# Kernel optimization log

Hardware: AMD Instinct MI355X
Metric: run time of the kernel (lower is better)

Reference implementation:

```python
import jax, jax.numpy as jnp
import numpy as np

SF, RES, TS = 8192, 40, 1  # sample freq, resolution (orders), time span (s)


def _eofft(inputs, rpm):
    """Engine-order FFT: per-sample zero-pad to length n_i = L + floor((RES*60/rpm_i - TS)*SF),
    FFT along time, keep first SF bins, take magnitude. Implemented as a fully batched
    Bluestein (chirp-z) transform so every sample uses the SAME fixed FFT size M,
    despite different logical FFT lengths n_i.
    """
    B, L, C = inputs.shape            # L == SF (required by the original .view)
    N = SF * TS                       # nonzero signal length after truncation (8192)
    K = SF                            # number of output bins kept (8192)
    M = int(2 ** np.ceil(np.log2(N + K - 1)))  # 16384, fixed batched FFT size

    x = inputs[:, :N, :]              # truncate, [B, N, C]
    pad = jnp.floor((RES * 60.0 / rpm - TS) * SF).astype(jnp.int32)  # [B]
    n = L + pad                       # per-sample DFT length n_i, [B] int32

    # Phases use exact integer m^2 mod 2n (exp(i*pi*q/n) has period 2n in q),
    # so float32 stays accurate even for large m.
    two_n = (2 * n)[:, None]                              # [B,1]
    nf = n.astype(jnp.float32)[:, None]                   # [B,1]

    # a[t] = x[t] * exp(-i*pi*t^2/n)
    t = jnp.arange(N, dtype=jnp.int32)
    a_phase = jnp.pi * ((t * t) % two_n).astype(jnp.float32) / nf      # [B,N]
    a = x.astype(jnp.complex64) * jnp.exp(-1j * a_phase)[:, :, None]   # [B,N,C]
    a = jnp.pad(a, ((0, 0), (0, M - N), (0, 0)))                       # [B,M,C]

    # b[m] = exp(+i*pi*m^2/n), laid out circularly: index m for m<K, index M-m for m=1..N-1
    m = jnp.arange(M, dtype=jnp.int32)
    mm = jnp.minimum(m, M - m)
    b_phase = jnp.pi * ((mm * mm) % two_n).astype(jnp.float32) / nf    # [B,M]
    b = jnp.exp(1j * b_phase)                                          # [B,M]

    # circular convolution via fixed-size FFTs (batched over B and C)
    conv = jnp.fft.ifft(jnp.fft.fft(a, axis=1) * jnp.fft.fft(b, axis=1)[:, :, None], axis=1)

    # X[k] = exp(-i*pi*k^2/n) * conv[k], k = 0..K-1
    k = jnp.arange(K, dtype=jnp.int32)
    k_phase = jnp.pi * ((k * k) % two_n).astype(jnp.float32) / nf      # [B,K]
    X = jnp.exp(-1j * k_phase)[:, :, None] * conv[:, :K, :]            # [B,K,C]
    return jnp.abs(X)                                                  # [B,SF,C] float32


def setup_inputs() -> dict:
    key = jax.random.key(0)
    k1, k2 = jax.random.split(key)
    B, L, C = 64, 8192, 8
    inputs = jax.random.normal(k1, (B, L, C), dtype=jnp.float32)
    rpm = jax.random.uniform(k2, (B,), dtype=jnp.float32, minval=600.0, maxval=2400.0)
    return {"inputs": inputs, "rpm": rpm}


def reference(inputs, rpm):
    return _eofft(inputs, rpm)
```

## Files before the change

### kernel.cpp

```cpp
#include <hip/hip_runtime.h>
#include <hip/hip_fp16.h>
#include <math.h>


static constexpr int Bn = 64;

#define PI_F 3.14159265358979323846f
#define TWO_PI_F 6.28318530717958647692f
#define R2_F 0.70710678118654752f

__device__ __forceinline__ int compute_n(float rpm) {
    return 8192 + (int)floorf((2400.0f / rpm - 1.0f) * 8192.0f);
}
__device__ __forceinline__ float2 cmul(float2 a, float2 b) {
    return make_float2(a.x*b.x - a.y*b.y, a.x*b.y + a.y*b.x);
}
__device__ __forceinline__ float2 cadd(float2 a, float2 b){ return make_float2(a.x+b.x, a.y+b.y); }
__device__ __forceinline__ float2 csub(float2 a, float2 b){ return make_float2(a.x-b.x, a.y-b.y); }
__device__ __forceinline__ float2 shflx1(float2 v) {
    return make_float2(__shfl_xor(v.x, 1, 64), __shfl_xor(v.y, 1, 64));
}
__device__ __forceinline__ int brev7(int x) { return (int)(__brev((unsigned)x) >> 25); }

#define BF(lo,hi,tw) { float2 _d = csub(lo,hi); lo = cadd(lo,hi); hi = cmul(_d, tw); }
#define BT(lo,hi,tw) { float2 _b = cmul(hi,tw); hi = csub(lo,_b); lo = cadd(lo,_b); }
#define SELC(r,c0,s0,c1,s1) ((r) ? make_float2(c1,s1) : make_float2(c0,s0))
#define IDX(u) ((u) + ((u) >> 4))

__device__ __forceinline__ float2 wtab(const float2* Whi, const float2* Wlo, int m) {
    return cmul(Whi[m >> 7], Wlo[m & 127]);
}

template<bool HZ>
__device__ __forceinline__ void difR(float2 v[8], float2* Lf, int p,
                                     const float2* sWhi) {
    float2 w1 = sWhi[p];
    float2 w2 = cmul(w1, w1);
    float2 w4 = cmul(w2, w2);
    float2 w1b = cmul(w1, make_float2(R2_F,-R2_F));
    float2 w1c = make_float2(w1.y, -w1.x);
    float2 w1d = cmul(w1, make_float2(-R2_F,-R2_F));
    float2 w2i = make_float2(w2.y, -w2.x);
    if (HZ) {
        v[4] = cmul(v[0], w1);
        v[5] = cmul(v[1], w1b);
        v[6] = cmul(v[2], w1c);
        v[7] = cmul(v[3], w1d);
    } else {
        BF(v[0],v[4], w1);
        BF(v[1],v[5], w1b);
        BF(v[2],v[6], w1c);
        BF(v[3],v[7], w1d);
    }
    BF(v[0],v[2], w2);  BF(v[1],v[3], w2i);
    BF(v[4],v[6], w2);  BF(v[5],v[7], w2i);
    BF(v[0],v[1], w4);  BF(v[2],v[3], w4);
    BF(v[4],v[5], w4);  BF(v[6],v[7], w4);
    #pragma unroll
    for (int q = 0; q < 8; ++q) Lf[IDX(p + 16*q)] = v[q];
    int bb = p >> 1, r = p & 1;
    #pragma unroll
    for (int s = 0; s < 8; ++s) v[s] = Lf[IDX(16*bb + r + 2*s)];
    BF(v[0],v[4], SELC(r, 1.f,0.f,                    0.92387953f,-0.38268343f));
    BF(v[1],v[5], SELC(r, 0.70710678f,-0.70710678f,   0.38268343f,-0.92387953f));
    BF(v[2],v[6], SELC(r, 0.f,-1.f,                  -0.38268343f,-0.92387953f));
    BF(v[3],v[7], SELC(r, -0.70710678f,-0.70710678f, -0.92387953f,-0.38268343f));
    BF(v[0],v[2], SELC(r, 1.f,0.f,  0.70710678f,-0.70710678f));
    BF(v[1],v[3], SELC(r, 0.f,-1.f, -0.70710678f,-0.70710678f));
    BF(v[4],v[6], SELC(r, 1.f,0.f,  0.70710678f,-0.70710678f));
    BF(v[5],v[7], SELC(r, 0.f,-1.f, -0.70710678f,-0.70710678f));
    #pragma unroll
    for (int s = 0; s < 8; s += 2) {
        float2 d = csub(v[s], v[s+1]);
        v[s] = cadd(v[s], v[s+1]);
        v[s+1] = r ? make_float2(d.y, -d.x) : d;
    }
    #pragma unroll
    for (int s = 0; s < 8; ++s) {
        float2 o = shflx1(v[s]);
        v[s] = r ? csub(o, v[s]) : cadd(v[s], o);
    }
}

template<bool HOUT>
__device__ __forceinline__ void ditR(float2 v[8], float2* Lf, int p,
                                     const float2* sWhi) {
    int bb = p >> 1, r = p & 1;
    #pragma unroll
    for (int s = 0; s < 8; ++s) {
        float2 o = shflx1(v[s]);
        v[s] = r ? csub(o, v[s]) : cadd(v[s], o);
    }
    #pragma unroll
    for (int s = 0; s < 8; s += 2) {
        float2 bq = v[s+1];
        if (r) bq = make_float2(-bq.y, bq.x);
        v[s+1] = csub(v[s], bq);
        v[s] = cadd(v[s], bq);
    }
    BT(v[0],v[2], SELC(r, 1.f,0.f,  0.70710678f,0.70710678f));
    BT(v[1],v[3], SELC(r, 0.f,1.f, -0.70710678f,0.70710678f));
    BT(v[4],v[6], SELC(r, 1.f,0.f,  0.70710678f,0.70710678f));
    BT(v[5],v[7], SELC(r, 0.f,1.f, -0.70710678f,0.70710678f));
    BT(v[0],v[4], SELC(r, 1.f,0.f,                   0.92387953f,0.38268343f));
    BT(v[1],v[5], SELC(r, 0.70710678f,0.70710678f,   0.38268343f,0.92387953f));
    BT(v[2],v[6], SELC(r, 0.f,1.f,                  -0.38268343f,0.92387953f));
    BT(v[3],v[7], SELC(r, -0.70710678f,0.70710678f, -0.92387953f,0.38268343f));
    #pragma unroll
    for (int s = 0; s < 8; ++s) Lf[IDX(16*bb + r + 2*s)] = v[s];
    #pragma unroll
    for (int q = 0; q < 8; ++q) v[q] = Lf[IDX(p + 16*q)];
    float2 w1 = make_float2(sWhi[p].x, -sWhi[p].y);
    float2 w2 = cmul(w1, w1);
    float2 w4 = cmul(w2, w2);
    float2 w2j = make_float2(-w2.y, w2.x);
    float2 w1b = cmul(w1, make_float2(R2_F, R2_F));
    float2 w1c = make_float2(-w1.y, w1.x);
    float2 w1d = cmul(w1, make_float2(-R2_F, R2_F));
    BT(v[0],v[1], w4); BT(v[2],v[3], w4);
    BT(v[4],v[5], w4); BT(v[6],v[7], w4);
    BT(v[0],v[2], w2);  BT(v[1],v[3], w2j);
    BT(v[4],v[6], w2);  BT(v[5],v[7], w2j);
    if (HOUT) {
        v[0] = cadd(v[0], cmul(v[4], w1));
        v[1] = cadd(v[1], cmul(v[5], w1b));
        v[2] = cadd(v[2], cmul(v[6], w1c));
        v[3] = cadd(v[3], cmul(v[7], w1d));
    } else {
        BT(v[0],v[4], w1);
        BT(v[1],v[5], w1b);
        BT(v[2],v[6], w1c);
        BT(v[3],v[7], w1d);
    }
}

__device__ __forceinline__ void load_tabs(float2* sWhi, float2* sWlo, int tid) {
    if (tid < 128) {
        float sn, cs; __sincosf(PI_F * (float)tid * (1.0f/64.0f), &sn, &cs);
        sWhi[tid] = make_float2(cs, -sn);
    } else if (tid < 256) {
        int m = tid - 128;
        float sn, cs; __sincosf(PI_F * (float)m * (1.0f/8192.0f), &sn, &cs);
        sWlo[m] = make_float2(cs, -sn);
    }
}

__global__ __launch_bounds__(256) void bhat_p1(const float* __restrict__ rpm,
                                               float2* __restrict__ w1c) {
    __shared__ float2 Lw[16 * 137];
    __shared__ float2 sWhi[128];
    __shared__ float2 sWlo[128];
    int tid = threadIdx.x;
    int g = tid >> 4, p = tid & 15;
    int bb = p >> 1, r = p & 1;
    int b = blockIdx.x >> 3;
    int t1_0 = (blockIdx.x & 7) << 4;

    load_tabs(sWhi, sWlo, tid);
    int n = compute_n(rpm[b]);
    int two_n = 2 * n;
    float inv_n = 1.0f / (float)n;
    #pragma unroll
    for (int i = 0; i < 8; ++i) {
        int l = i * 256 + tid;
        int t2 = l >> 4, c = l & 15;
        int t = (t1_0 + c) + (t2 << 7);
        int mm = min(t, 16384 - t);
        int ph = (mm * mm) % two_n;
        float sn, cs; __sincosf(PI_F * (float)ph * inv_n, &sn, &cs);
        Lw[c * 137 + IDX(t2)] = make_float2(cs, sn);
    }
    __syncthreads();
    float2 v[8];
    #pragma unroll
    for (int q = 0; q < 8; ++q) v[q] = Lw[g * 137 + IDX(p + 16*q)];
    difR<false>(v, Lw + g * 137, p, sWhi);
    __syncthreads();
    {
        int t1 = t1_0 + g;
        int k2base = brev7(16*bb + r);
        float2 cur = wtab(sWhi, sWlo, t1 * k2base);
        float2 w8  = wtab(sWhi, sWlo, 8 * t1);
        #pragma unroll
        for (int e = 0; e < 8; ++e) {
            const int s = ((e & 1) << 2) | (e & 2) | ((e & 4) >> 2);
            Lw[(16*bb + r + 2*s) * 17 + g] = cmul(v[s], cur);
            cur = cmul(cur, w8);
        }
    }
    __syncthreads();
    {
        float2* wb = w1c + ((size_t)b << 14) + t1_0;
        #pragma unroll
        for (int i = 0; i < 8; ++i) {
            int l = i * 256 + tid;
            int j = l >> 4, w = l & 15;
            wb[(j << 7) + w] = Lw[j * 17 + w];
        }
    }
}

__global__ __launch_bounds__(256) void k1(const float* __restrict__ x,
                                          const float* __restrict__ rpm,
                                          __half2* __restrict__ w1) {
    __shared__ float2 Lw[16 * 137];
    __shared__ float2 chirpT[128];
    __shared__ float2 sWhi[128];
    __shared__ float2 sWlo[128];
    int tid = threadIdx.x;
    int g = tid >> 4, p = tid & 15;
    int bb = p >> 1, r = p & 1;
    int b = blockIdx.x >> 6;
    int t1_0 = (blockIdx.x & 63) << 1;

    load_tabs(sWhi, sWlo, tid);
    int n = compute_n(rpm[b]);
    int two_n = 2 * n;
    float inv_n = 1.0f / (float)n;
    if (tid < 128) {
        int t2 = tid >> 1, t1l = tid & 1;
        int t = t1_0 + t1l + (t2 << 7);
        int ph = (t * t) % two_n;
        float sn, cs; __sincosf(PI_F * (float)ph * inv_n, &sn, &cs);
        chirpT[tid] = make_float2(cs, -sn);
    }
    __syncthreads();
    {
        const float2* xb2 = (const float2*)(x + ((size_t)b << 16));
        #pragma unroll
        for (int i = 0; i < 2; ++i) {
            int l = i * 256 + tid;
            int t2 = l >> 3, w = l & 7;
            int t1l = w >> 2, cp = w & 3;
            float2 xv = xb2[(size_t)(t1_0 + t1l + (t2 << 7)) * 4 + cp];
            float2 u = chirpT[t2 * 2 + t1l];
            int c = t1l * 8 + cp * 2;
            Lw[c * 137 + IDX(t2)]       = make_float2(xv.x * u.x, xv.x * u.y);
            Lw[(c + 1) * 137 + IDX(t2)] = make_float2(xv.y * u.x, xv.y * u.y);
        }
    }
    __syncthreads();
    float2 v[8];
    #pragma unroll
    for (int q = 0; q < 4; ++q) v[q] = Lw[g * 137 + IDX(p + 16*q)];
    difR<true>(v, Lw + g * 137, p, sWhi);
    __syncthreads();
    {
        int t1 = t1_0 + (g >> 3);
        int k2base = brev7(16*bb + r);
        float2 cur = wtab(sWhi, sWlo, t1 * k2base);
        float2 w8  = wtab(sWhi, sWlo, 8 * t1);
        #pragma unroll
        for (int e = 0; e < 8; ++e) {
            const int s = ((e & 1) << 2) | (e & 2) | ((e & 4) >> 2);
            Lw[(16*bb + r + 2*s) * 17 + g] = cmul(v[s], cur);
            cur = cmul(cur, w8);
        }
    }
    __syncthreads();
    {
        __half2* wb = w1 + ((size_t)b << 17) + (t1_0 << 3);
        #pragma unroll
        for (int i = 0; i < 8; ++i) {
            int l = i * 256 + tid;
            int j = l >> 4, w = l & 15;
            wb[((size_t)j << 10) + w] = __float22half2_rn(Lw[j * 17 + w]);
        }
    }
}

__global__ __launch_bounds__(512) void k2(const __half2* __restrict__ w1,
                                          const float2* __restrict__ w1c,
                                          __half2* __restrict__ s2) {
    __shared__ float2 Lw[32 * 137];
    __shared__ float2 Wsc[4 * 137];
    __shared__ float2 sWhi[128];
    __shared__ float2 sWlo[128];
    int tid = threadIdx.x;
    int g = tid >> 4, p = tid & 15;
    int b = blockIdx.x >> 5;
    int j0 = (blockIdx.x & 31) << 2;

    load_tabs(sWhi, sWlo, tid);
    float2 vb[8];
    if (g < 4) {
        const float2* wc = w1c + ((size_t)b << 14) + ((size_t)(j0 + g) << 7);
        #pragma unroll
        for (int q = 0; q < 8; ++q) vb[q] = wc[p + 16*q];
    }
    {
        const __half2* rb = w1 + ((size_t)b << 17) + ((size_t)j0 << 10);
        #pragma unroll
        for (int i = 0; i < 8; ++i) {
            int l = i * 512 + tid;
            int jl = l >> 10, t1 = (l >> 3) & 127, ch = l & 7;
            Lw[(jl * 8 + ch) * 137 + IDX(t1)] = __half22float2(rb[l]);
        }
    }
    __syncthreads();
    if (g < 4) {
        difR<false>(vb, Wsc + g * 137, p, sWhi);
        #pragma unroll
        for (int s = 0; s < 8; ++s) Wsc[g * 137 + s * 17 + p] = vb[s];
    }
    float2* Lf = Lw + g * 137;
    float2 v[8];
    #pragma unroll
    for (int q = 0; q < 8; ++q) v[q] = Lf[IDX(p + 16*q)];
    difR<false>(v, Lf, p, sWhi);
    __syncthreads();
    {
        int jl = g >> 3;
        #pragma unroll
        for (int s = 0; s < 8; ++s) v[s] = cmul(v[s], Wsc[jl * 137 + s * 17 + p]);
    }
    ditR<false>(v, Lf, p, sWhi);
    int j = j0 + (g >> 3);
    int k2v = brev7(j);
    __syncthreads();
    {
        float2 cur = wtab(sWhi, sWlo, k2v * p);
        float2 w16 = wtab(sWhi, sWlo, 16 * k2v);
        #pragma unroll
        for (int q = 0; q < 8; ++q) {
            float2 tw = make_float2(cur.x * (1.0f/16384.0f), -cur.y * (1.0f/16384.0f));
            Lw[(p + 16*q) * 33 + g] = cmul(v[q], tw);
            cur = cmul(cur, w16);
        }
    }
    __syncthreads();
    {
        __half2* sb = s2 + ((size_t)b << 17) + (j0 << 3);
        #pragma unroll
        for (int i = 0; i < 8; ++i) {
            int l = i * 512 + tid;
            int t1 = l >> 5, w = l & 31;
            sb[((size_t)t1 << 10) + w] = __float22half2_rn(Lw[t1 * 33 + w]);
        }
    }
}

__global__ __launch_bounds__(256) void k3(const __half2* __restrict__ s2,
                                          float* __restrict__ outF) {
    __shared__ float2 Lw[16 * 137];
    __shared__ float2 sWhi[128];
    __shared__ float2 sWlo[128];
    int tid = threadIdx.x;
    int g = tid >> 4, p = tid & 15;
    int bb = p >> 1, r = p & 1;
    int b = blockIdx.x >> 6;
    int t1_0 = (blockIdx.x & 63) << 1;

    load_tabs(sWhi, sWlo, tid);
    {
        const __half2* rb = s2 + ((size_t)b << 17) + ((size_t)t1_0 << 10);
        #pragma unroll
        for (int i = 0; i < 8; ++i) {
            int l = i * 256 + tid;
            int t1l = l >> 10, j = (l >> 3) & 127, ch = l & 7;
            Lw[(t1l * 8 + ch) * 137 + IDX(j)] = __half22float2(rb[l]);
        }
    }
    __syncthreads();
    float2 v[8];
    {
        float2* Lf = Lw + g * 137;
        #pragma unroll
        for (int s = 0; s < 8; ++s) v[s] = Lf[IDX(16*bb + r + 2*s)];
        ditR<true>(v, Lf, p, sWhi);
    }
    __syncthreads();
    float* Lsf = (float*)Lw;
    #pragma unroll
    for (int q = 0; q < 4; ++q) {
        float2 z = v[q];
        Lsf[(p + 16*q) * 20 + g] = sqrtf(z.x*z.x + z.y*z.y);
    }
    __syncthreads();
    {
        float* ob = outF + ((size_t)b << 16) + (t1_0 << 3);
        #pragma unroll
        for (int i = 0; i < 4; ++i) {
            int l = i * 256 + tid;
            int t2 = l >> 4, w = l & 15;
            ob[((size_t)t2 << 10) + w] = Lsf[t2 * 20 + w];
        }
    }
}

extern "C" void kernel_launch(void* const* d_in, const int* in_sizes, int n_in,
                              void* d_out, int out_size, void* d_ws, size_t ws_size,
                              hipStream_t stream) {
    const float* x   = (const float*)d_in[0];
    const float* rpm = (const float*)d_in[1];
    float* outF = (float*)d_out;
    __half2* w1  = (__half2*)d_ws;
    __half2* s2  = w1 + (size_t)Bn * 131072;
    float2* w1c  = (float2*)(s2 + (size_t)Bn * 131072);

    bhat_p1<<<Bn * 8, 256, 0, stream>>>(rpm, w1c);
    k1<<<Bn * 64, 256, 0, stream>>>(x, rpm, w1);
    k2<<<Bn * 32, 512, 0, stream>>>(w1, w1c, s2);
    k3<<<Bn * 64, 256, 0, stream>>>(s2, outF);
}
```

Measured before the change: 76.28 us.

## Merge chirp-FFT kernel into k1 and widen global accesses to float4

New measurement: 70.48 us. 7.6% less time.

```diff
diff --git a/kernel.cpp b/kernel.cpp
--- a/kernel.cpp
+++ b/kernel.cpp
@@ -21,6 +21,17 @@
     return make_float2(__shfl_xor(v.x, 1, 64), __shfl_xor(v.y, 1, 64));
 }
 __device__ __forceinline__ int brev7(int x) { return (int)(__brev((unsigned)x) >> 25); }
+
+__device__ __forceinline__ float f2h_bits(float2 a) {
+    union { __half2 h; float f; } u;
+    u.h = __float22half2_rn(a);
+    return u.f;
+}
+__device__ __forceinline__ float2 h2f_bits(float w) {
+    union { float f; __half2 h; } u;
+    u.f = w;
+    return __half22float2(u.h);
+}
 
 #define BF(lo,hi,tw) { float2 _d = csub(lo,hi); lo = cadd(lo,hi); hi = cmul(_d, tw); }
 #define BT(lo,hi,tw) { float2 _b = cmul(hi,tw); hi = csub(lo,_b); lo = cadd(lo,_b); }
@@ -145,64 +156,10 @@
     }
 }
 
-__global__ __launch_bounds__(256) void bhat_p1(const float* __restrict__ rpm,
-                                               float2* __restrict__ w1c) {
-    __shared__ float2 Lw[16 * 137];
-    __shared__ float2 sWhi[128];
-    __shared__ float2 sWlo[128];
-    int tid = threadIdx.x;
-    int g = tid >> 4, p = tid & 15;
-    int bb = p >> 1, r = p & 1;
-    int b = blockIdx.x >> 3;
-    int t1_0 = (blockIdx.x & 7) << 4;
-
-    load_tabs(sWhi, sWlo, tid);
-    int n = compute_n(rpm[b]);
-    int two_n = 2 * n;
-    float inv_n = 1.0f / (float)n;
-    #pragma unroll
-    for (int i = 0; i < 8; ++i) {
-        int l = i * 256 + tid;
-        int t2 = l >> 4, c = l & 15;
-        int t = (t1_0 + c) + (t2 << 7);
-        int mm = min(t, 16384 - t);
-        int ph = (mm * mm) % two_n;
-        float sn, cs; __sincosf(PI_F * (float)ph * inv_n, &sn, &cs);
-        Lw[c * 137 + IDX(t2)] = make_float2(cs, sn);
-    }
-    __syncthreads();
-    float2 v[8];
-    #pragma unroll
-    for (int q = 0; q < 8; ++q) v[q] = Lw[g * 137 + IDX(p + 16*q)];
-    difR<false>(v, Lw + g * 137, p, sWhi);
-    __syncthreads();
-    {
-        int t1 = t1_0 + g;
-        int k2base = brev7(16*bb + r);
-        float2 cur = wtab(sWhi, sWlo, t1 * k2base);
-        float2 w8  = wtab(sWhi, sWlo, 8 * t1);
-        #pragma unroll
-        for (int e = 0; e < 8; ++e) {
-            const int s = ((e & 1) << 2) | (e & 2) | ((e & 4) >> 2);
-            Lw[(16*bb + r + 2*s) * 17 + g] = cmul(v[s], cur);
-            cur = cmul(cur, w8);
-        }
-    }
-    __syncthreads();
-    {
-        float2* wb = w1c + ((size_t)b << 14) + t1_0;
-        #pragma unroll
-        for (int i = 0; i < 8; ++i) {
-            int l = i * 256 + tid;
-            int j = l >> 4, w = l & 15;
-            wb[(j << 7) + w] = Lw[j * 17 + w];
-        }
-    }
-}
-
-__global__ __launch_bounds__(256) void k1(const float* __restrict__ x,
-                                          const float* __restrict__ rpm,
-                                          __half2* __restrict__ w1) {
+__global__ __launch_bounds__(256) void k1b(const float* __restrict__ x,
+                                           const float* __restrict__ rpm,
+                                           __half2* __restrict__ w1,
+                                           float2* __restrict__ w1c) {
     __shared__ float2 Lw[16 * 137];
     __shared__ float2 chirpT[128];
     __shared__ float2 sWhi[128];
@@ -210,10 +167,61 @@
     int tid = threadIdx.x;
     int g = tid >> 4, p = tid & 15;
     int bb = p >> 1, r = p & 1;
-    int b = blockIdx.x >> 6;
-    int t1_0 = (blockIdx.x & 63) << 1;
 
     load_tabs(sWhi, sWlo, tid);
+
+    if (blockIdx.x < Bn * 8) {
+        int b = blockIdx.x >> 3;
+        int t1_0 = (blockIdx.x & 7) << 4;
+        int n = compute_n(rpm[b]);
+        int two_n = 2 * n;
+        float inv_n = 1.0f / (float)n;
+        #pragma unroll
+        for (int i = 0; i < 8; ++i) {
+            int l = i * 256 + tid;
+            int t2 = l >> 4, c = l & 15;
+            int t = (t1_0 + c) + (t2 << 7);
+            int mm = min(t, 16384 - t);
+            int ph = (mm * mm) % two_n;
+            float sn, cs; __sincosf(PI_F * (float)ph * inv_n, &sn, &cs);
+            Lw[c * 137 + IDX(t2)] = make_float2(cs, sn);
+        }
+        __syncthreads();
+        float2 v[8];
+        #pragma unroll
+        for (int q = 0; q < 8; ++q) v[q] = Lw[g * 137 + IDX(p + 16*q)];
+        difR<false>(v, Lw + g * 137, p, sWhi);
+        __syncthreads();
+        {
+            int t1 = t1_0 + g;
+            int k2base = brev7(16*bb + r);
+            float2 cur = wtab(sWhi, sWlo, t1 * k2base);
+            float2 w8  = wtab(sWhi, sWlo, 8 * t1);
+            #pragma unroll
+            for (int e = 0; e < 8; ++e) {
+                const int s = ((e & 1) << 2) | (e & 2) | ((e & 4) >> 2);
+                Lw[(16*bb + r + 2*s) * 17 + g] = cmul(v[s], cur);
+                cur = cmul(cur, w8);
+            }
+        }
+        __syncthreads();
+        {
+            float4* wb4 = (float4*)(w1c + ((size_t)b << 14) + t1_0);
+            #pragma unroll
+            for (int i = 0; i < 4; ++i) {
+                int l = i * 256 + tid;
+                int j = l >> 3, w2 = l & 7;
+                float2 a0 = Lw[j * 17 + w2*2];
+                float2 a1 = Lw[j * 17 + w2*2 + 1];
+                wb4[(size_t)j * 64 + w2] = make_float4(a0.x, a0.y, a1.x, a1.y);
+            }
+        }
+        return;
+    }
+
+    int bid = blockIdx.x - Bn * 8;
+    int b = bid >> 6;
+    int t1_0 = (bid & 63) << 1;
     int n = compute_n(rpm[b]);
     int two_n = 2 * n;
     float inv_n = 1.0f / (float)n;
@@ -226,18 +234,18 @@
     }
     __syncthreads();
     {
-        const float2* xb2 = (const float2*)(x + ((size_t)b << 16));
-        #pragma unroll
-        for (int i = 0; i < 2; ++i) {
-            int l = i * 256 + tid;
-            int t2 = l >> 3, w = l & 7;
-            int t1l = w >> 2, cp = w & 3;
-            float2 xv = xb2[(size_t)(t1_0 + t1l + (t2 << 7)) * 4 + cp];
-            float2 u = chirpT[t2 * 2 + t1l];
-            int c = t1l * 8 + cp * 2;
-            Lw[c * 137 + IDX(t2)]       = make_float2(xv.x * u.x, xv.x * u.y);
-            Lw[(c + 1) * 137 + IDX(t2)] = make_float2(xv.y * u.x, xv.y * u.y);
-        }
+        const float4* xb4 = (const float4*)(x + ((size_t)b << 16));
+        int l = tid;
+        int t2 = l >> 2, rem = l & 3;
+        int t1l = rem >> 1, cp = rem & 1;
+        int t = t1_0 + t1l + (t2 << 7);
+        float4 xv = xb4[(size_t)t * 2 + cp];
+        float2 u = chirpT[t2 * 2 + t1l];
+        int c = t1l * 8 + cp * 4;
+        Lw[c * 137 + IDX(t2)]       = make_float2(xv.x * u.x, xv.x * u.y);
+        Lw[(c + 1) * 137 + IDX(t2)] = make_float2(xv.y * u.x, xv.y * u.y);
+        Lw[(c + 2) * 137 + IDX(t2)] = make_float2(xv.z * u.x, xv.z * u.y);
+        Lw[(c + 3) * 137 + IDX(t2)] = make_float2(xv.w * u.x, xv.w * u.y);
     }
     __syncthreads();
     float2 v[8];
@@ -259,12 +267,17 @@
     }
     __syncthreads();
     {
-        __half2* wb = w1 + ((size_t)b << 17) + (t1_0 << 3);
-        #pragma unroll
-        for (int i = 0; i < 8; ++i) {
+        float4* wb4 = (float4*)(w1 + ((size_t)b << 17) + (t1_0 << 3));
+        #pragma unroll
+        for (int i = 0; i < 2; ++i) {
             int l = i * 256 + tid;
-            int j = l >> 4, w = l & 15;
-            wb[((size_t)j << 10) + w] = __float22half2_rn(Lw[j * 17 + w]);
+            int j = l >> 2, w4 = l & 3;
+            float4 val;
+            val.x = f2h_bits(Lw[j * 17 + w4*4 + 0]);
+            val.y = f2h_bits(Lw[j * 17 + w4*4 + 1]);
+            val.z = f2h_bits(Lw[j * 17 + w4*4 + 2]);
+            val.w = f2h_bits(Lw[j * 17 + w4*4 + 3]);
+            wb4[(size_t)j * 256 + w4] = val;
         }
     }
 }
@@ -289,12 +302,17 @@
         for (int q = 0; q < 8; ++q) vb[q] = wc[p + 16*q];
     }
     {
-        const __half2* rb = w1 + ((size_t)b << 17) + ((size_t)j0 << 10);
-        #pragma unroll
-        for (int i = 0; i < 8; ++i) {
+        const float4* rb4 = (const float4*)(w1 + ((size_t)b << 17) + ((size_t)j0 << 10));
+        #pragma unroll
+        for (int i = 0; i < 2; ++i) {
             int l = i * 512 + tid;
-            int jl = l >> 10, t1 = (l >> 3) & 127, ch = l & 7;
-            Lw[(jl * 8 + ch) * 137 + IDX(t1)] = __half22float2(rb[l]);
+            int jl = l >> 8, rem = l & 255, t1 = rem >> 1, ch4 = rem & 1;
+            float4 d = rb4[l];
+            int c = jl * 8 + ch4 * 4;
+            Lw[(c + 0) * 137 + IDX(t1)] = h2f_bits(d.x);
+            Lw[(c + 1) * 137 + IDX(t1)] = h2f_bits(d.y);
+            Lw[(c + 2) * 137 + IDX(t1)] = h2f_bits(d.z);
+            Lw[(c + 3) * 137 + IDX(t1)] = h2f_bits(d.w);
         }
     }
     __syncthreads();
@@ -330,12 +348,17 @@
     }
     __syncthreads();
     {
-        __half2* sb = s2 + ((size_t)b << 17) + (j0 << 3);
-        #pragma unroll
-        for (int i = 0; i < 8; ++i) {
+        float4* sb4 = (float4*)(s2 + ((size_t)b << 17) + (j0 << 3));
+        #pragma unroll
+        for (int i = 0; i < 2; ++i) {
             int l = i * 512 + tid;
-            int t1 = l >> 5, w = l & 31;
-            sb[((size_t)t1 << 10) + w] = __float22half2_rn(Lw[t1 * 33 + w]);
+            int t1 = l >> 3, w4 = l & 7;
+            float4 val;
+            val.x = f2h_bits(Lw[t1 * 33 + w4*4 + 0]);
+            val.y = f2h_bits(Lw[t1 * 33 + w4*4 + 1]);
+            val.z = f2h_bits(Lw[t1 * 33 + w4*4 + 2]);
+            val.w = f2h_bits(Lw[t1 * 33 + w4*4 + 3]);
+            sb4[(size_t)t1 * 256 + w4] = val;
         }
     }
 }
@@ -353,12 +376,17 @@
 
     load_tabs(sWhi, sWlo, tid);
     {
-        const __half2* rb = s2 + ((size_t)b << 17) + ((size_t)t1_0 << 10);
-        #pragma unroll
-        for (int i = 0; i < 8; ++i) {
+        const float4* rb4 = (const float4*)(s2 + ((size_t)b << 17) + ((size_t)t1_0 << 10));
+        #pragma unroll
+        for (int i = 0; i < 2; ++i) {
             int l = i * 256 + tid;
-            int t1l = l >> 10, j = (l >> 3) & 127, ch = l & 7;
-            Lw[(t1l * 8 + ch) * 137 + IDX(j)] = __half22float2(rb[l]);
+            int t1l = l >> 8, rem = l & 255, j = rem >> 1, ch4 = rem & 1;
+            float4 d = rb4[l];
+            int c = t1l * 8 + ch4 * 4;
+            Lw[(c + 0) * 137 + IDX(j)] = h2f_bits(d.x);
+            Lw[(c + 1) * 137 + IDX(j)] = h2f_bits(d.y);
+            Lw[(c + 2) * 137 + IDX(j)] = h2f_bits(d.z);
+            Lw[(c + 3) * 137 + IDX(j)] = h2f_bits(d.w);
         }
     }
     __syncthreads();
@@ -378,13 +406,11 @@
     }
     __syncthreads();
     {
-        float* ob = outF + ((size_t)b << 16) + (t1_0 << 3);
-        #pragma unroll
-        for (int i = 0; i < 4; ++i) {
-            int l = i * 256 + tid;
-            int t2 = l >> 4, w = l & 15;
-            ob[((size_t)t2 << 10) + w] = Lsf[t2 * 20 + w];
-        }
+        float4* ob4 = (float4*)(outF + ((size_t)b << 16) + (t1_0 << 3));
+        int t2 = tid >> 2, t1l = (tid >> 1) & 1, ch4 = tid & 1;
+        int base = t2 * 20 + t1l * 8 + ch4 * 4;
+        float4 val = make_float4(Lsf[base], Lsf[base + 1], Lsf[base + 2], Lsf[base + 3]);
+        ob4[t2 * 256 + t1l * 2 + ch4] = val;
     }
 }
 
@@ -398,8 +424,7 @@
     __half2* s2  = w1 + (size_t)Bn * 131072;
     float2* w1c  = (float2*)(s2 + (size_t)Bn * 131072);
 
-    bhat_p1<<<Bn * 8, 256, 0, stream>>>(rpm, w1c);
-    k1<<<Bn * 64, 256, 0, stream>>>(x, rpm, w1);
+    k1b<<<Bn * 8 + Bn * 64, 256, 0, stream>>>(x, rpm, w1, w1c);
     k2<<<Bn * 32, 512, 0, stream>>>(w1, w1c, s2);
     k3<<<Bn * 64, 256, 0, stream>>>(s2, outF);
 }
```
